# Performance work log

Measured on AMD Instinct MI355X. Metric: run time of the kernel, lower is better.

## Reference

```python
import jax, jax.numpy as jnp
import numpy as np

GROUP = 32  # MX block size (scales buffer is in_features // 32) == hadamard_group_size
# E2M1 (FP4) representable magnitudes and rounding midpoints
_GRID = jnp.array([0.0, 0.5, 1.0, 1.5, 2.0, 3.0, 4.0, 6.0], dtype=jnp.float32)
_MIDS = jnp.array([0.25, 0.75, 1.25, 1.75, 2.5, 3.5, 5.0], dtype=jnp.float32)


def _hadamard(n):
    # Sylvester construction, scaled by n**-0.5 (orthonormal), as in pre_forward
    H = np.array([[1.0]], dtype=np.float32)
    while H.shape[0] < n:
        H = np.block([[H, H], [H, -H]])
    return jnp.asarray(H / np.sqrt(n), dtype=jnp.float32)


def _mxfp4_qdq(v):
    # v: [..., GROUP]. Shared E8M0 scale per group: 2^(floor(log2(amax)) - emax_fp4),
    # emax for E2M1 is 2 (max magnitude 6.0). Elements rounded onto the FP4 grid.
    amax = jnp.max(jnp.abs(v), axis=-1, keepdims=True)
    e = jnp.floor(jnp.log2(jnp.maximum(amax, 2.0 ** -126))) - 2.0
    scale = jnp.exp2(jnp.clip(e, -127.0, 127.0))
    s = v / scale
    a = jnp.minimum(jnp.abs(s), 6.0)
    idx = jnp.sum(a[..., None] > _MIDS, axis=-1)  # nearest FP4 magnitude
    q = _GRID[idx] * jnp.sign(s)
    return q * scale


def _rotate_quant(t, H):
    # group last dim into blocks of GROUP, Hadamard-rotate each block, MXFP4 quant-dequant
    shp = t.shape
    tg = t.reshape(*shp[:-1], shp[-1] // GROUP, GROUP)
    tg = jnp.einsum('...gk,kj->...gj', tg, H)
    return _mxfp4_qdq(tg).reshape(shp)


def setup_inputs() -> dict:
    key = jax.random.key(0)
    k1, k2, k3 = jax.random.split(key, 3)
    T, K, N = 8192, 4096, 4096  # tokens, in_features, out_features
    x = jax.random.normal(k1, (T, K), dtype=jnp.float32)
    weight = jax.random.normal(k2, (N, K), dtype=jnp.float32) * 0.02
    bias = jax.random.normal(k3, (N,), dtype=jnp.float32) * 0.01
    hadamard_matrix = _hadamard(GROUP)
    return {"x": x, "weight": weight, "bias": bias, "hadamard_matrix": hadamard_matrix}


def reference(x, weight, bias, hadamard_matrix):
    # FPQuant forward (MXFP4 forward, master weights): rotate+quantize both
    # activations and weights per 32-wide group, then dequantized GEMM + bias.
    xq = _rotate_quant(x, hadamard_matrix)            # [T, K]
    wq = _rotate_quant(weight, hadamard_matrix)       # [N, K]
    return xq @ wq.T + bias                           # [T, N]
```

## Files before the change

kernel.cpp:

```cpp
#include <hip/hip_runtime.h>
#include <hip/hip_bf16.h>

typedef __attribute__((ext_vector_type(8))) short bf16x8;
typedef __attribute__((ext_vector_type(4))) float f32x4;

#define AS1C(p) ((const __attribute__((address_space(1))) void*)(p))
#define AS3(p)  ((__attribute__((address_space(3))) void*)(p))

__global__ void rotquant_kernel(const float* __restrict__ in,
                                unsigned short* __restrict__ out, int ngroups) {
    int g = blockIdx.x * blockDim.x + threadIdx.x;
    if (g >= ngroups) return;

    const float4* p = (const float4*)(in + (size_t)g * 32);
    float v[32];
#pragma unroll
    for (int i = 0; i < 8; ++i) {
        float4 q = p[i];
        v[4 * i + 0] = q.x; v[4 * i + 1] = q.y;
        v[4 * i + 2] = q.z; v[4 * i + 3] = q.w;
    }

#pragma unroll
    for (int s = 1; s < 32; s <<= 1) {
#pragma unroll
        for (int i = 0; i < 32; ++i) {
            if (!(i & s)) {
                float a = v[i], b = v[i + s];
                v[i] = a + b;
                v[i + s] = a - b;
            }
        }
    }

    const float INV = 0.17677669529663687f;
    float amax = 0.f;
#pragma unroll
    for (int i = 0; i < 32; ++i) {
        v[i] *= INV;
        amax = fmaxf(amax, fabsf(v[i]));
    }

    int ex = (int)(__float_as_uint(amax) >> 23) - 127;
    if (ex < -126) ex = -126;
    int e = ex - 2;
    if (e < -127) e = -127;
    float scale  = __uint_as_float((unsigned)(e + 127) << 23);
    float rscale = __uint_as_float((unsigned)(127 - e) << 23);

    __attribute__((aligned(16))) unsigned short o[32];
#pragma unroll
    for (int i = 0; i < 32; ++i) {
        float s = v[i] * rscale;
        float a = fminf(fabsf(s), 6.0f);
        float q = a > 0.25f ? (a > 0.75f ? (a > 1.25f ? (a > 1.75f ?
                  (a > 2.5f ? (a > 3.5f ? (a > 5.0f ? 6.f : 4.f) : 3.f) : 2.f)
                  : 1.5f) : 1.f) : 0.5f) : 0.f;
        float r = copysignf(q, s) * scale;
        o[i] = (unsigned short)(__float_as_uint(r) >> 16);
    }

    unsigned short* op = out + (size_t)g * 32;
#pragma unroll
    for (int i = 0; i < 4; ++i)
        ((bf16x8*)op)[i] = *(const bf16x8*)&o[8 * i];
}

#define GBM 128
#define GBN 128
#define GBK 32

__global__ void gemm_bt_kernel(const unsigned short* __restrict__ A,
                               const unsigned short* __restrict__ B,
                               const float* __restrict__ bias,
                               float* __restrict__ C,
                               int M, int N, int K) {
    __shared__ unsigned short sA[GBM * GBK];
    __shared__ unsigned short sB[GBN * GBK];

    int nbn = N / GBN;
    int nwg = (M / GBM) * nbn;
    int bid = blockIdx.x;
    int swz;
    if ((nwg & 7) == 0) {
        int cpx = nwg >> 3;
        swz = (bid & 7) * cpx + (bid >> 3);
    } else {
        swz = bid;
    }
    int bm = swz / nbn, bn = swz % nbn;

    int t = threadIdx.x;
    int lane = t & 63;
    int wid = t >> 6;
    int wr = wid >> 1, wc = wid & 1;
    int fr = lane & 15, fq = lane >> 4;

    f32x4 acc[4][4] = {};

    const unsigned short* gA = A + (size_t)bm * GBM * K + (size_t)(t >> 2) * K + (t & 3) * 8;
    const unsigned short* gB = B + (size_t)bn * GBN * K + (size_t)(t >> 2) * K + (t & 3) * 8;
    unsigned short* sAp = sA + t * 8;
    unsigned short* sBp = sB + t * 8;
    const size_t rowStep = (size_t)64 * K;

    for (int kb = 0; kb < K; kb += GBK) {
        __syncthreads();
        __builtin_amdgcn_global_load_lds(AS1C(gA + kb),           AS3(sAp),        16, 0, 0);
        __builtin_amdgcn_global_load_lds(AS1C(gA + kb + rowStep), AS3(sAp + 2048), 16, 0, 0);
        __builtin_amdgcn_global_load_lds(AS1C(gB + kb),           AS3(sBp),        16, 0, 0);
        __builtin_amdgcn_global_load_lds(AS1C(gB + kb + rowStep), AS3(sBp + 2048), 16, 0, 0);
        __syncthreads();

        bf16x8 af[4], bfr[4];
#pragma unroll
        for (int m = 0; m < 4; ++m)
            af[m] = *(const bf16x8*)&sA[(wr * 64 + m * 16 + fr) * GBK + fq * 8];
#pragma unroll
        for (int n = 0; n < 4; ++n)
            bfr[n] = *(const bf16x8*)&sB[(wc * 64 + n * 16 + fr) * GBK + fq * 8];

#pragma unroll
        for (int m = 0; m < 4; ++m)
#pragma unroll
            for (int n = 0; n < 4; ++n)
                acc[m][n] = __builtin_amdgcn_mfma_f32_16x16x32_bf16(
                    af[m], bfr[n], acc[m][n], 0, 0, 0);
    }

    int row0 = bm * GBM + wr * 64 + fq * 4;
    int col0 = bn * GBN + wc * 64 + fr;
#pragma unroll
    for (int m = 0; m < 4; ++m) {
#pragma unroll
        for (int n = 0; n < 4; ++n) {
            int c = col0 + n * 16;
            float bv = bias[c];
#pragma unroll
            for (int j = 0; j < 4; ++j) {
                int r = row0 + m * 16 + j;
                C[(size_t)r * N + c] = acc[m][n][j] + bv;
            }
        }
    }
}

extern "C" void kernel_launch(void* const* d_in, const int* in_sizes, int n_in,
                              void* d_out, int out_size, void* d_ws, size_t ws_size,
                              hipStream_t stream) {
    const float* x    = (const float*)d_in[0];
    const float* w    = (const float*)d_in[1];
    const float* bias = (const float*)d_in[2];

    int N = in_sizes[2];
    int K = in_sizes[1] / N;
    int M = in_sizes[0] / K;

    unsigned short* xq = (unsigned short*)d_ws;
    unsigned short* wq = xq + (size_t)M * K;

    int ngx = (int)(((size_t)M * K) / 32);
    int ngw = (int)(((size_t)N * K) / 32);

    rotquant_kernel<<<dim3((ngx + 255) / 256), dim3(256), 0, stream>>>(x, xq, ngx);
    rotquant_kernel<<<dim3((ngw + 255) / 256), dim3(256), 0, stream>>>(w, wq, ngw);

    int grid = (M / GBM) * (N / GBN);
    gemm_bt_kernel<<<dim3(grid), dim3(256), 0, stream>>>(xq, wq, bias, (float*)d_out, M, N, K);
}
```

Before: 583.7 us.

## Split each Hadamard group across 8 lanes with shuffle butterflies in rotquant

The rotate-quantize kernel now assigns each 32-element group to 8 lanes, each holding a float4. The first two butterfly stages run in-register and the last three use xor shuffles, and the group amax is reduced with shuffles. A grid-stride loop with a capped grid replaces one-thread-per-group. The aim is fully coalesced loads and stores and lower register pressure than the old 32-float-per-thread layout, at the cost of extra shuffle instructions.

```diff
diff --git a/kernel.cpp b/kernel.cpp
--- a/kernel.cpp
+++ b/kernel.cpp
@@ -8,62 +8,70 @@
 #define AS3(p)  ((__attribute__((address_space(3))) void*)(p))
 
 __global__ void rotquant_kernel(const float* __restrict__ in,
-                                unsigned short* __restrict__ out, int ngroups) {
-    int g = blockIdx.x * blockDim.x + threadIdx.x;
-    if (g >= ngroups) return;
+                                unsigned short* __restrict__ out,
+                                size_t nslots ) {
+    const int j = threadIdx.x & 7;
+    const size_t stride = (size_t)gridDim.x * blockDim.x;
+    const float INV = 0.17677669529663687f;
 
-    const float4* p = (const float4*)(in + (size_t)g * 32);
-    float v[32];
+    for (size_t s = (size_t)blockIdx.x * blockDim.x + threadIdx.x;
+         s < nslots; s += stride) {
+        const size_t g = s >> 3;
+        float4 v = *(const float4*)(in + g * 32 + j * 4);
+
+        {
+            float a = v.x, b = v.y, c = v.z, d = v.w;
+            v.x = a + b; v.y = a - b; v.z = c + d; v.w = c - d;
+        }
+        {
+            float a = v.x, b = v.y, c = v.z, d = v.w;
+            v.x = a + c; v.z = a - c; v.y = b + d; v.w = b - d;
+        }
 #pragma unroll
-    for (int i = 0; i < 8; ++i) {
-        float4 q = p[i];
-        v[4 * i + 0] = q.x; v[4 * i + 1] = q.y;
-        v[4 * i + 2] = q.z; v[4 * i + 3] = q.w;
-    }
-
-#pragma unroll
-    for (int s = 1; s < 32; s <<= 1) {
-#pragma unroll
-        for (int i = 0; i < 32; ++i) {
-            if (!(i & s)) {
-                float a = v[i], b = v[i + s];
-                v[i] = a + b;
-                v[i + s] = a - b;
+        for (int m = 1; m <= 4; m <<= 1) {
+            float px = __shfl_xor(v.x, m, 64);
+            float py = __shfl_xor(v.y, m, 64);
+            float pz = __shfl_xor(v.z, m, 64);
+            float pw = __shfl_xor(v.w, m, 64);
+            if (j & m) {
+                v.x = px - v.x; v.y = py - v.y;
+                v.z = pz - v.z; v.w = pw - v.w;
+            } else {
+                v.x = v.x + px; v.y = v.y + py;
+                v.z = v.z + pz; v.w = v.w + pw;
             }
         }
+
+        v.x *= INV; v.y *= INV; v.z *= INV; v.w *= INV;
+
+        float amax = fmaxf(fmaxf(fabsf(v.x), fabsf(v.y)),
+                           fmaxf(fabsf(v.z), fabsf(v.w)));
+#pragma unroll
+        for (int m = 1; m <= 4; m <<= 1)
+            amax = fmaxf(amax, __shfl_xor(amax, m, 64));
+
+        int ex = (int)(__float_as_uint(amax) >> 23) - 127;
+        if (ex < -126) ex = -126;
+        int e = ex - 2;
+        if (e < -127) e = -127;
+        float scale  = __uint_as_float((unsigned)(e + 127) << 23);
+        float rscale = __uint_as_float((unsigned)(127 - e) << 23);
+
+        ushort4 o;
+        float elems[4] = {v.x, v.y, v.z, v.w};
+        unsigned short* po = (unsigned short*)&o;
+#pragma unroll
+        for (int i = 0; i < 4; ++i) {
+            float sv = elems[i] * rscale;
+            float a = fminf(fabsf(sv), 6.0f);
+            float q = a > 0.25f ? (a > 0.75f ? (a > 1.25f ? (a > 1.75f ?
+                      (a > 2.5f ? (a > 3.5f ? (a > 5.0f ? 6.f : 4.f) : 3.f) : 2.f)
+                      : 1.5f) : 1.f) : 0.5f) : 0.f;
+            float r = copysignf(q, sv) * scale;
+            po[i] = (unsigned short)(__float_as_uint(r) >> 16);
+        }
+        *(ushort4*)(out + g * 32 + j * 4) = o;
     }
-
-    const float INV = 0.17677669529663687f;
-    float amax = 0.f;
-#pragma unroll
-    for (int i = 0; i < 32; ++i) {
-        v[i] *= INV;
-        amax = fmaxf(amax, fabsf(v[i]));
-    }
-
-    int ex = (int)(__float_as_uint(amax) >> 23) - 127;
-    if (ex < -126) ex = -126;
-    int e = ex - 2;
-    if (e < -127) e = -127;
-    float scale  = __uint_as_float((unsigned)(e + 127) << 23);
-    float rscale = __uint_as_float((unsigned)(127 - e) << 23);
-
-    __attribute__((aligned(16))) unsigned short o[32];
-#pragma unroll
-    for (int i = 0; i < 32; ++i) {
-        float s = v[i] * rscale;
-        float a = fminf(fabsf(s), 6.0f);
-        float q = a > 0.25f ? (a > 0.75f ? (a > 1.25f ? (a > 1.75f ?
-                  (a > 2.5f ? (a > 3.5f ? (a > 5.0f ? 6.f : 4.f) : 3.f) : 2.f)
-                  : 1.5f) : 1.f) : 0.5f) : 0.f;
-        float r = copysignf(q, s) * scale;
-        o[i] = (unsigned short)(__float_as_uint(r) >> 16);
-    }
-
-    unsigned short* op = out + (size_t)g * 32;
-#pragma unroll
-    for (int i = 0; i < 4; ++i)
-        ((bf16x8*)op)[i] = *(const bf16x8*)&o[8 * i];
 }
 
 #define GBM 128
@@ -159,11 +167,14 @@
     unsigned short* xq = (unsigned short*)d_ws;
     unsigned short* wq = xq + (size_t)M * K;
 
-    int ngx = (int)(((size_t)M * K) / 32);
-    int ngw = (int)(((size_t)N * K) / 32);
+    size_t nsx = ((size_t)M * K / 32) * 8;
+    size_t nsw = ((size_t)N * K / 32) * 8;
 
-    rotquant_kernel<<<dim3((ngx + 255) / 256), dim3(256), 0, stream>>>(x, xq, ngx);
-    rotquant_kernel<<<dim3((ngw + 255) / 256), dim3(256), 0, stream>>>(w, wq, ngw);
+    int gx = (int)(((nsx + 255) / 256) < 4096 ? ((nsx + 255) / 256) : 4096);
+    int gw = (int)(((nsw + 255) / 256) < 4096 ? ((nsw + 255) / 256) : 4096);
+
+    rotquant_kernel<<<dim3(gx), dim3(256), 0, stream>>>(x, xq, nsx);
+    rotquant_kernel<<<dim3(gw), dim3(256), 0, stream>>>(w, wq, nsw);
 
     int grid = (M / GBM) * (N / GBN);
     gemm_bt_kernel<<<dim3(grid), dim3(256), 0, stream>>>(xq, wq, bias, (float*)d_out, M, N, K);
```

Measured after the change: 587.0 us. About the same (+0.6%).
